# Performance work log

Measured on AMD Instinct MI355X. Metric: run time of the kernel, lower is better.

Reference implementation:

```python
import jax, jax.numpy as jnp
import numpy as np
from jax import lax
from jax.scipy.special import logsumexp

B, T, Lc = 64, 512, 16
DW, CD, NF, KS, H, K, CV = 300, 50, 100, 3, 256, 9, 100
SCALE = 0.05


def setup_inputs() -> dict:
    key = jax.random.key(0)
    ks = jax.random.split(key, 20)
    f32 = jnp.float32
    return {
        'word_embs': jax.random.normal(ks[0], (B, T, DW), f32),
        'chars': jax.random.randint(ks[1], (B, T, Lc), 0, CV),
        'lengths': jax.random.randint(ks[2], (B,), T // 2, T + 1).astype(jnp.int32),
        'tags': jax.random.randint(ks[3], (B, T), 0, K),
        'fin_W': jax.random.normal(ks[4], (DW, DW), f32) * SCALE,
        'fin_b': jnp.zeros((DW,), f32),
        'char_emb': jax.random.normal(ks[5], (CV, CD), f32) * SCALE,
        'conv_W': jax.random.normal(ks[6], (KS, CD, NF), f32) * SCALE,  # (W, In, Out)
        'conv_b': jnp.zeros((NF,), f32),
        'Wih_f': jax.random.normal(ks[7], (4 * H, DW + NF), f32) * SCALE,
        'Whh_f': jax.random.normal(ks[8], (4 * H, H), f32) * SCALE,
        'b_f': jnp.zeros((4 * H,), f32),
        'Wih_b': jax.random.normal(ks[9], (4 * H, DW + NF), f32) * SCALE,
        'Whh_b': jax.random.normal(ks[10], (4 * H, H), f32) * SCALE,
        'b_b': jnp.zeros((4 * H,), f32),
        'out_W': jax.random.normal(ks[11], (2 * H, K), f32) * SCALE,
        'out_b': jnp.zeros((K,), f32),
        'trans': jax.random.normal(ks[12], (K, K), f32) * SCALE,
        'start_trans': jax.random.normal(ks[13], (K,), f32) * SCALE,
        'end_trans': jax.random.normal(ks[14], (K,), f32) * SCALE,
    }


def _lstm_scan(x, mask, Wih, Whh, b):
    # x: [B,T,D], mask: [B,T] bool -> outputs [B,T,H] (zeros at padding)
    xT = jnp.swapaxes(x, 0, 1)              # [T,B,D]
    mT = jnp.swapaxes(mask, 0, 1)           # [T,B]
    pre = jnp.einsum('tbd,gd->tbg', xT, Wih) + b  # precompute input part [T,B,4H]
    h0 = jnp.zeros((x.shape[0], Whh.shape[1]), x.dtype)

    def step(carry, inp):
        h, c = carry
        px, m = inp
        g = px + h @ Whh.T
        i, f, gg, o = jnp.split(g, 4, axis=-1)  # pytorch gate order i,f,g,o
        c_new = jax.nn.sigmoid(f) * c + jax.nn.sigmoid(i) * jnp.tanh(gg)
        h_new = jax.nn.sigmoid(o) * jnp.tanh(c_new)
        m = m[:, None]
        h2 = jnp.where(m, h_new, h)
        c2 = jnp.where(m, c_new, c)
        return (h2, c2), h2 * m

    _, hs = lax.scan(step, (h0, h0), (pre, mT))
    return jnp.swapaxes(hs, 0, 1)


def _reverse_by_length(x, lengths):
    # reverse the valid prefix of each sequence (padding stays at the end)
    t = jnp.arange(x.shape[1])
    rev = jnp.where(t[None, :] < lengths[:, None], lengths[:, None] - 1 - t[None, :], t[None, :])
    return jnp.take_along_axis(x, rev[:, :, None], axis=1)


def _crf_forward(logits, tags, mask, trans, start_trans, end_trans):
    # torchcrf-style log-likelihood; returns scalar sum over batch
    eT = jnp.swapaxes(logits, 0, 1)  # [T,B,K]
    mT = jnp.swapaxes(mask, 0, 1).astype(logits.dtype)  # [T,B]
    bidx = jnp.arange(logits.shape[0])
    # numerator: gold path score
    score = start_trans[tags[:, 0]] + eT[0][bidx, tags[:, 0]]

    def nstep(carry, inp):
        sc, prev = carry
        e, tg, m = inp
        step_sc = trans[prev, tg] + e[bidx, tg]
        sc = sc + m * step_sc
        prev = jnp.where(m > 0, tg, prev)
        return (sc, prev), None

    tT = jnp.swapaxes(tags, 0, 1)
    (score, last_tag), _ = lax.scan(nstep, (score, tags[:, 0]), (eT[1:], tT[1:], mT[1:]))
    score = score + end_trans[last_tag]
    # denominator: log-partition via forward algorithm
    alpha = start_trans[None, :] + eT[0]

    def fstep(a, inp):
        e, m = inp
        nxt = logsumexp(a[:, :, None] + trans[None, :, :] + e[:, None, :], axis=1)
        return jnp.where(m[:, None] > 0, nxt, a), None

    alpha, _ = lax.scan(fstep, alpha, (eT[1:], mT[1:]))
    Z = logsumexp(alpha + end_trans[None, :], axis=-1)
    return jnp.sum(score - Z)


def _viterbi(logits, mask, trans, start_trans, end_trans):
    eT = jnp.swapaxes(logits, 0, 1)  # [T,B,K]
    mT = jnp.swapaxes(mask, 0, 1)    # [T,B] bool
    Ktags = logits.shape[-1]
    ident = jnp.arange(Ktags)[None, :]

    def vstep(a, inp):
        e, m = inp
        cand = a[:, :, None] + trans[None, :, :]   # [B, K_prev, K_cur]
        bp = jnp.argmax(cand, axis=1)
        nxt = jnp.max(cand, axis=1) + e
        a2 = jnp.where(m[:, None], nxt, a)
        bp = jnp.where(m[:, None], bp, ident)       # identity backptr at padding
        return a2, bp

    alpha, bps = lax.scan(vstep, start_trans[None, :] + eT[0], (eT[1:], mT[1:]))
    last = jnp.argmax(alpha + end_trans[None, :], axis=-1)

    def bstep(tag, bp):
        prev = jnp.take_along_axis(bp, tag[:, None], axis=1)[:, 0]
        return prev, tag

    tag0, tail = lax.scan(bstep, last, bps, reverse=True)  # tail[t] = tag at time t+1
    path = jnp.concatenate([tag0[:, None], jnp.swapaxes(tail, 0, 1)], axis=1)  # [B,T]
    return path * mask  # zero-pad like zero_pad(preds)


def reference(word_embs, chars, lengths, tags, fin_W, fin_b, char_emb, conv_W, conv_b,
              Wih_f, Whh_f, b_f, Wih_b, Whh_b, b_b, out_W, out_b,
              trans, start_trans, end_trans):
    mask = jnp.arange(T)[None, :] < lengths[:, None]  # [B,T]
    # 1) word embeddings through finetune linear
    we = word_embs @ fin_W.T + fin_b
    # 2) char CNN: embed -> conv1d over chars -> relu -> max-pool
    ce = char_emb[chars].reshape(B * T, Lc, CD)
    conv = lax.conv_general_dilated(ce, conv_W, (1,), 'SAME',
                                    dimension_numbers=('NWC', 'WIO', 'NWC')) + conv_b
    char_feat = jnp.max(jax.nn.relu(conv), axis=1).reshape(B, T, NF)
    # 3) concat; 4) BiLSTM (dropout=0 / eval mode)
    x = jnp.concatenate([we, char_feat], axis=-1)
    h_fwd = _lstm_scan(x, mask, Wih_f, Whh_f, b_f)
    x_rev = _reverse_by_length(x, lengths)
    h_bwd = _reverse_by_length(_lstm_scan(x_rev, mask, Wih_b, Whh_b, b_b), lengths)
    lstm_out = jnp.concatenate([h_fwd, h_bwd], axis=-1)  # [B,T,2H]
    # 5) linear head; 6-7) CRF loss + viterbi decode
    logits = lstm_out @ out_W + out_b  # [B,T,K]
    loss = -_crf_forward(logits, tags, mask, trans, start_trans, end_trans)
    preds = _viterbi(logits, mask, trans, start_trans, end_trans)
    return loss, preds
```

## Files before the change

### kernel.cpp

```cpp
#include <hip/hip_runtime.h>


__device__ __forceinline__ float sigf(float x){ return 1.0f/(1.0f + expf(-x)); }

__global__ void pack_weights(const float* __restrict__ Wih_f, const float* __restrict__ Wih_b,
                             const float* __restrict__ Whh_f, const float* __restrict__ Whh_b,
                             const float* __restrict__ fin_W,
                             float4* __restrict__ Wp_f, float4* __restrict__ Wp_b,
                             float4* __restrict__ WT_f, float4* __restrict__ WT_b,
                             float* __restrict__ finWT){
  int stride = gridDim.x*blockDim.x;
  for (int idx = blockIdx.x*blockDim.x + threadIdx.x; idx < 425872; idx += stride){
    if (idx < 204800){
      int i2 = idx; const float* W = Wih_f; float4* P = Wp_f;
      if (i2 >= 102400){ i2 -= 102400; W = Wih_b; P = Wp_b; }
      int d = i2 >> 8, j = i2 & 255;
      P[i2] = make_float4(W[j*400+d], W[(j+256)*400+d], W[(j+512)*400+d], W[(j+768)*400+d]);
    } else if (idx < 335872){
      int i2 = idx - 204800; const float* W = Whh_f; float4* P = WT_f;
      if (i2 >= 65536){ i2 -= 65536; W = Whh_b; P = WT_b; }
      int d = i2 >> 8, j = i2 & 255;
      P[i2] = make_float4(W[j*256+d], W[(j+256)*256+d], W[(j+512)*256+d], W[(j+768)*256+d]);
    } else {
      int i2 = idx - 335872;
      int d = i2 / 300, j = i2 - d*300;
      finWT[d*304 + j] = fin_W[j*300 + d];
    }
  }
}

__global__ __launch_bounds__(256) void embed_kernel(const float* __restrict__ we_in,
      const float* __restrict__ finWT, const float* __restrict__ finb, float* __restrict__ x){
  __shared__ float embT[300*16];
  int tok0 = blockIdx.x * 16;
  for (int idx = threadIdx.x; idx < 4800; idx += 256){
    int tt = idx / 300, d = idx - tt*300;
    embT[d*16 + tt] = we_in[(size_t)tok0*300 + idx];
  }
  __syncthreads();
  for (int j = threadIdx.x; j < 300; j += 256){
    float bias = finb[j];
    float acc[16];
#pragma unroll
    for (int k2=0;k2<16;k2++) acc[k2]=bias;
    const float4* e4 = (const float4*)embT;
#pragma unroll 4
    for (int d=0; d<300; d++){
      float w = finWT[d*304 + j];
      float4 a = e4[d*4+0], b2 = e4[d*4+1], c2 = e4[d*4+2], d2 = e4[d*4+3];
      acc[0]+=a.x*w;  acc[1]+=a.y*w;  acc[2]+=a.z*w;  acc[3]+=a.w*w;
      acc[4]+=b2.x*w; acc[5]+=b2.y*w; acc[6]+=b2.z*w; acc[7]+=b2.w*w;
      acc[8]+=c2.x*w; acc[9]+=c2.y*w; acc[10]+=c2.z*w;acc[11]+=c2.w*w;
      acc[12]+=d2.x*w;acc[13]+=d2.y*w;acc[14]+=d2.z*w;acc[15]+=d2.w*w;
    }
#pragma unroll
    for (int k2=0;k2<16;k2++) x[(size_t)(tok0+k2)*400 + j] = acc[k2];
  }
}

__global__ __launch_bounds__(256) void char_kernel(const int* __restrict__ chars,
      const float* __restrict__ char_emb, const float* __restrict__ convW,
      const float* __restrict__ convb, float* __restrict__ x){
  __shared__ float ce2[8*952];
  __shared__ int chs[128];
  int tok0 = blockIdx.x * 8;
  int tid = threadIdx.x;
  if (tid < 128) chs[tid] = chars[(size_t)tok0*16 + tid];
  __syncthreads();
  for (int idx = tid; idx < 7200; idx += 256){
    int tok = idx / 900; int r = idx - tok*900;
    int w1 = r / 50; int c = r - w1*50;
    float v = 0.f;
    if (w1 >= 1 && w1 <= 16) v = char_emb[chs[tok*16 + (w1-1)]*50 + c];
    ce2[tok*952 + c*19 + w1] = v;
  }
  __syncthreads();
  for (int p = tid; p < 800; p += 256){
    int tok = p / 100, f = p - tok*100;
    float s[16];
#pragma unroll
    for (int w=0; w<16; w++) s[w] = 0.f;
    const float* cebase = ce2 + tok*952;
    for (int c=0; c<50; c++){
      float cr[18];
#pragma unroll
      for (int i=0;i<18;i++) cr[i] = cebase[c*19+i];
#pragma unroll
      for (int k2=0;k2<3;k2++){
        float wv = convW[(k2*50+c)*100 + f];
#pragma unroll
        for (int w=0;w<16;w++) s[w] += cr[w+k2]*wv;
      }
    }
    float m = s[0];
#pragma unroll
    for (int w=1;w<16;w++) m = fmaxf(m, s[w]);
    m = fmaxf(0.f, m + convb[f]);
    x[(size_t)(tok0+tok)*400 + 300 + f] = m;
  }
}

__global__ __launch_bounds__(256) void pre_gemm(const float* __restrict__ x,
     const float4* __restrict__ Wp_f, const float4* __restrict__ Wp_b,
     const float* __restrict__ b_f, const float* __restrict__ b_b,
     const int* __restrict__ lengths,
     float4* __restrict__ pre_f, float4* __restrict__ pre_b,
     int t0, int log2CH){
  int dir = blockIdx.z;
  const float4* Wp = dir ? Wp_b : Wp_f;
  const float* bias = dir ? b_b : b_f;
  float4* pre = dir ? pre_b : pre_f;
  int tok0 = blockIdx.x * 64;
  int j0 = blockIdx.y * 64;
  __shared__ float As[16][68];
  __shared__ float4 Bs[4][16][16];
  __shared__ int rows_s[64];
  int tid = threadIdx.x;
  int tx = tid & 15, ty = tid >> 4;
  if (tid < 64){
    int tok = tok0 + tid;
    int b = tok >> log2CH;
    int trel = tok - (b << log2CH);
    int t = t0 + trel;
    int row;
    if (dir == 0) row = t;
    else { int len = lengths[b]; int pr = len - 1 - t; row = pr < 0 ? 0 : pr; }
    rows_s[tid] = b*512 + row;
  }
  float4 acc[4][4];
#pragma unroll
  for (int s2=0;s2<4;s2++){
    int j = j0 + tx*4 + s2;
    float4 bj = make_float4(bias[j], bias[j+256], bias[j+512], bias[j+768]);
#pragma unroll
    for (int r=0;r<4;r++) acc[r][s2] = bj;
  }
  __syncthreads();
  int tokA = tid >> 2, kqA = tid & 3;
  int jjB = tid & 63,  kbB = tid >> 6;
  float4 aReg; float4 bReg[4];
  {
    aReg = *(const float4*)&x[(size_t)rows_s[tokA]*400 + 0 + kqA*4];
#pragma unroll
    for (int rr=0;rr<4;rr++) bReg[rr] = Wp[(size_t)(0 + kbB + rr*4)*256 + j0 + jjB];
  }
  for (int kt=0; kt<25; ++kt){
    As[kqA*4+0][tokA] = aReg.x;
    As[kqA*4+1][tokA] = aReg.y;
    As[kqA*4+2][tokA] = aReg.z;
    As[kqA*4+3][tokA] = aReg.w;
#pragma unroll
    for (int rr=0;rr<4;rr++) Bs[jjB&3][kbB+rr*4][jjB>>2] = bReg[rr];
    __syncthreads();
    if (kt < 24){
      int k0n = (kt+1)*16;
      aReg = *(const float4*)&x[(size_t)rows_s[tokA]*400 + k0n + kqA*4];
#pragma unroll
      for (int rr=0;rr<4;rr++) bReg[rr] = Wp[(size_t)(k0n + kbB + rr*4)*256 + j0 + jjB];
    }
#pragma unroll
    for (int kk=0; kk<16; ++kk){
      float a[4];
#pragma unroll
      for (int r=0;r<4;r++) a[r] = As[kk][ty*4+r];
#pragma unroll
      for (int s2=0;s2<4;s2++){
        float4 b4 = Bs[s2][kk][tx];
#pragma unroll
        for (int r=0;r<4;r++){
          acc[r][s2].x += a[r]*b4.x;
          acc[r][s2].y += a[r]*b4.y;
          acc[r][s2].z += a[r]*b4.z;
          acc[r][s2].w += a[r]*b4.w;
        }
      }
    }
    __syncthreads();
  }
#pragma unroll
  for (int r=0;r<4;r++){
    int tok = tok0 + ty*4 + r;
    int bb = tok >> log2CH;
    int tr = tok - (bb << log2CH);
#pragma unroll
    for (int s2=0;s2<4;s2++){
      pre[(size_t)(bb*128 + tr)*256 + j0 + tx*4 + s2] = acc[r][s2];
    }
  }
}

#define NRD 24
#define NLD 8
#define NSTREAM (64 - NRD - NLD)

#define OFF_WLDS 0
#define OFF_PART 131072
#define OFF_OWS  143360
#define OFF_H    152576
#define POOL_SZ  154624
#define PG_AS    0
#define PG_BS    4352
#define PG_ROWS  12544
#define PG_STRIDE 12800

__global__ __launch_bounds__(1024, 1)
void fused_scan_pre(const float4* __restrict__ prec_f, const float4* __restrict__ prec_b,
     const float4* __restrict__ pren_f, float4* __restrict__ pren_f_w,
     float4* __restrict__ pren_b_w,
     const float4* __restrict__ WT_f, const float4* __restrict__ WT_b,
     const float4* __restrict__ Wp_f, const float4* __restrict__ Wp_b,
     const float* __restrict__ b_f, const float* __restrict__ b_b,
     const float* __restrict__ x, const int* __restrict__ lengths,
     const float* __restrict__ outW,
     float* __restrict__ logits_f, float* __restrict__ logits_b,
     float* __restrict__ st_h, float* __restrict__ st_c,
     int t0, int nsteps, int t0n, int do_pre){
  __shared__ __align__(16) char smem[POOL_SZ];
  int wid = blockIdx.x;
  int tid = threadIdx.x;
  if (wid < 128){
    int dir = wid & 1;
    int b = wid >> 1;
    int len = lengths[b];
    if (len <= t0) return;
    const float4* pre = (dir ? prec_b : prec_f) + (size_t)b*128*256;
    const float4* WT = dir ? WT_b : WT_f;
    float* lg = (dir ? logits_b : logits_f) + (size_t)b*512*9;
    float4* wlds = (float4*)(smem + OFF_WLDS);
    float4* part = (float4*)(smem + OFF_PART);
    float*  oWs  = (float*)(smem + OFF_OWS);
    float*  hbuf = (float*)(smem + OFF_H);
    int j = tid & 255, q = tid >> 8;
    for (int i = tid; i < 2304; i += 1024) oWs[i] = outW[dir*2304 + i];
    for (int i = tid; i < 4*NLD*256; i += 1024){
      int qq = i >> 11;
      int rr = i & (NLD*256 - 1);
      int dl = rr >> 8, jj = rr & 255;
      wlds[(qq*NLD + dl)*256 + jj] = WT[(size_t)(qq*64 + NRD + dl)*256 + jj];
    }
    const float4* WTq = WT + (size_t)q*64*256;
    float4 wreg[NRD];
#pragma unroll
    for (int r=0; r<NRD; ++r) wreg[r] = WTq[(size_t)r*256 + j];
    float c = 0.f;
    if (t0 == 0){
      if (tid < 256) hbuf[tid] = 0.f;
    } else {
      if (tid < 256) hbuf[tid] = st_h[(dir*64+b)*256 + tid];
      if (q == 0) c = st_c[(dir*64+b)*256 + j];
    }
    __syncthreads();
    int tend = len < t0+nsteps ? len : t0+nsteps;
    const float4* WTs = WTq + (size_t)(NRD+NLD)*256 + j;
    int cur = 0;
    for (int t=t0; t<tend; ++t){
      const float* hc = hbuf + (cur << 8);
      const float* hq = hc + (q << 6);
      float4 p0;
      if (q == 0) p0 = pre[(size_t)(t - t0)*256 + j];
      float4 acc = make_float4(0.f,0.f,0.f,0.f);
#pragma unroll 8
      for (int s=0; s<NSTREAM; ++s){
        float hv = hq[NRD+NLD+s];
        float4 w = WTs[(size_t)s*256];
        acc.x += w.x*hv; acc.y += w.y*hv; acc.z += w.z*hv; acc.w += w.w*hv;
      }
#pragma unroll
      for (int r=0; r<NRD; ++r){
        float hv = hq[r];
        float4 w = wreg[r];
        acc.x += w.x*hv; acc.y += w.y*hv; acc.z += w.z*hv; acc.w += w.w*hv;
      }
#pragma unroll
      for (int l=0; l<NLD; ++l){
        float hv = hq[NRD+l];
        float4 w = wlds[(q*NLD + l)*256 + j];
        acc.x += w.x*hv; acc.y += w.y*hv; acc.z += w.z*hv; acc.w += w.w*hv;
      }
      if (q) part[((q-1)<<8) + j] = acc;
      if (t > t0 && tid < 576){
        int pprev = dir ? (len - t) : (t - 1);
        int k = tid >> 6, l = tid & 63;
        float s = hc[l]*oWs[l*9+k] + hc[l+64]*oWs[(l+64)*9+k]
                + hc[l+128]*oWs[(l+128)*9+k] + hc[l+192]*oWs[(l+192)*9+k];
#pragma unroll
        for (int o=32; o; o>>=1) s += __shfl_down(s, o, 64);
        if (l == 0) lg[pprev*9 + k] = s;
      }
      __syncthreads();
      if (q == 0){
        float4 p1 = part[j], p2 = part[256+j], p3 = part[512+j];
        float gi = acc.x + p0.x + p1.x + p2.x + p3.x;
        float gf = acc.y + p0.y + p1.y + p2.y + p3.y;
        float gg = acc.z + p0.z + p1.z + p2.z + p3.z;
        float go = acc.w + p0.w + p1.w + p2.w + p3.w;
        c = sigf(gf)*c + sigf(gi)*tanhf(gg);
        float h = sigf(go)*tanhf(c);
        hbuf[((cur^1)<<8) + j] = h;
      }
      __syncthreads();
      cur ^= 1;
    }
    const float* hc = hbuf + (cur << 8);
    if (tid < 576){
      int plast = dir ? (len - tend) : (tend - 1);
      int k = tid >> 6, l = tid & 63;
      float s = hc[l]*oWs[l*9+k] + hc[l+64]*oWs[(l+64)*9+k]
              + hc[l+128]*oWs[(l+128)*9+k] + hc[l+192]*oWs[(l+192)*9+k];
#pragma unroll
      for (int o=32; o; o>>=1) s += __shfl_down(s, o, 64);
      if (l == 0) lg[plast*9 + k] = s;
    }
    if (tid < 256) st_h[(dir*64+b)*256 + tid] = hc[tid];
    if (q == 0) st_c[(dir*64+b)*256 + j] = c;
  } else {
    if (!do_pre) return;
    int w = wid - 128;
    int g = tid >> 8, lt = tid & 255;
    char* gp = smem + g*PG_STRIDE;
    float (*As)[68] = (float(*)[68])(gp + PG_AS);
    float4* Bsl = (float4*)(gp + PG_BS);
    int* rows = (int*)(gp + PG_ROWS);
    int tx = lt & 15, ty4 = (lt >> 4) * 4;
    int tokA = lt >> 2, kqA = lt & 3;
    int uB = lt & 31, kbB = lt >> 5;
    for (int s=0; s<4; ++s){
      int tix = s*512 + g*128 + w;
      int dir = tix & 1;
      int jh = (tix >> 1) & 7;
      int tokT = tix >> 4;
      int j0u = jh * 32;
      int tok0 = tokT * 64;
      const float4* Wp = dir ? Wp_b : Wp_f;
      const float* bias = dir ? b_b : b_f;
      float4* pren = dir ? pren_b_w : pren_f_w;
      __syncthreads();
      if (lt < 64){
        int tok = tok0 + lt;
        int bb = tok >> 7, trel = tok & 127;
        int t = t0n + trel; if (t > 511) t = 511;
        int row;
        if (dir == 0) row = t;
        else { int len = lengths[bb]; int pr = len - 1 - t; row = pr < 0 ? 0 : pr; }
        rows[lt] = bb*512 + row;
      }
      float4 acc[4][2];
#pragma unroll
      for (int s2=0;s2<2;s2++){
        int u = j0u + tx + s2*16;
        float4 bj = make_float4(bias[u], bias[u+256], bias[u+512], bias[u+768]);
#pragma unroll
        for (int r=0;r<4;r++) acc[r][s2] = bj;
      }
      __syncthreads();
      for (int kt=0; kt<25; ++kt){
        int k0 = kt*16;
        {
          const float* xr = x + (size_t)rows[tokA]*400 + k0 + kqA*4;
          float4 av = *(const float4*)xr;
          As[kqA*4+0][tokA]=av.x; As[kqA*4+1][tokA]=av.y;
          As[kqA*4+2][tokA]=av.z; As[kqA*4+3][tokA]=av.w;
          Bsl[kbB*32 + uB]     = Wp[(size_t)(k0+kbB)*256 + j0u + uB];
          Bsl[(kbB+8)*32 + uB] = Wp[(size_t)(k0+kbB+8)*256 + j0u + uB];
        }
        __syncthreads();
#pragma unroll 4
        for (int kk=0; kk<16; ++kk){
          float a0 = As[kk][ty4+0], a1 = As[kk][ty4+1], a2 = As[kk][ty4+2], a3 = As[kk][ty4+3];
          float4 b0 = Bsl[kk*32 + tx], b1 = Bsl[kk*32 + tx + 16];
          acc[0][0].x += a0*b0.x; acc[0][0].y += a0*b0.y; acc[0][0].z += a0*b0.z; acc[0][0].w += a0*b0.w;
          acc[1][0].x += a1*b0.x; acc[1][0].y += a1*b0.y; acc[1][0].z += a1*b0.z; acc[1][0].w += a1*b0.w;
          acc[2][0].x += a2*b0.x; acc[2][0].y += a2*b0.y; acc[2][0].z += a2*b0.z; acc[2][0].w += a2*b0.w;
          acc[3][0].x += a3*b0.x; acc[3][0].y += a3*b0.y; acc[3][0].z += a3*b0.z; acc[3][0].w += a3*b0.w;
          acc[0][1].x += a0*b1.x; acc[0][1].y += a0*b1.y; acc[0][1].z += a0*b1.z; acc[0][1].w += a0*b1.w;
          acc[1][1].x += a1*b1.x; acc[1][1].y += a1*b1.y; acc[1][1].z += a1*b1.z; acc[1][1].w += a1*b1.w;
          acc[2][1].x += a2*b1.x; acc[2][1].y += a2*b1.y; acc[2][1].z += a2*b1.z; acc[2][1].w += a2*b1.w;
          acc[3][1].x += a3*b1.x; acc[3][1].y += a3*b1.y; acc[3][1].z += a3*b1.z; acc[3][1].w += a3*b1.w;
        }
        __syncthreads();
      }
#pragma unroll
      for (int r=0;r<4;r++){
        int tok = tok0 + ty4 + r;
        pren[(size_t)tok*256 + j0u + tx]      = acc[r][0];
        pren[(size_t)tok*256 + j0u + tx + 16] = acc[r][1];
      }
    }
  }
}

__global__ __launch_bounds__(64) void crf_viterbi_kernel(const float* __restrict__ logits_f,
     const float* __restrict__ logits_b, const float* __restrict__ outb_,
     const int* __restrict__ tags, const int* __restrict__ lengths,
     const float* __restrict__ trans, const float* __restrict__ start_trans,
     const float* __restrict__ end_trans, float* __restrict__ loss_partial,
     float* __restrict__ preds){
  int wid = blockIdx.x;
  int is_crf = wid < 64 ? 1 : 0;
  int b = is_crf ? wid : wid - 64;
  int len = lengths[b];
  int tid = threadIdx.x;
  __shared__ float e_s[4608];
  __shared__ float tr[81];
  __shared__ float alpha[9];
  __shared__ int tg[512];
  __shared__ unsigned char bp[4608];
  const float* lf = logits_f + (size_t)b*4608;
  const float* lb = logits_b + (size_t)b*4608;
  for (int i=tid; i<4608; i+=64){
    int k = i - (i/9)*9;
    e_s[i] = lf[i] + lb[i] + outb_[k];
  }
  for (int i=tid; i<81; i+=64) tr[i] = trans[i];
  if (is_crf){
    for (int i=tid; i<512; i+=64) tg[i] = tags[b*512 + i];
    __syncthreads();
    if (tid < 9) alpha[tid] = start_trans[tid] + e_s[tid];
    __syncthreads();
    for (int t=1; t<len; ++t){
      float nxt = 0.f;
      if (tid < 9){
        float v[9];
#pragma unroll
        for (int j2=0;j2<9;j2++) v[j2] = alpha[j2] + tr[j2*9+tid];
        float m = v[0];
#pragma unroll
        for (int j2=1;j2<9;j2++) m = fmaxf(m, v[j2]);
        float ssum = 0.f;
#pragma unroll
        for (int j2=0;j2<9;j2++) ssum += expf(v[j2]-m);
        nxt = m + logf(ssum) + e_s[t*9+tid];
      }
      __syncthreads();
      if (tid < 9) alpha[tid] = nxt;
      __syncthreads();
    }
    if (tid == 0){
      float m = alpha[0] + end_trans[0];
      for (int k2=1;k2<9;k2++) m = fmaxf(m, alpha[k2]+end_trans[k2]);
      float ssum = 0.f;
      for (int k2=0;k2<9;k2++) ssum += expf(alpha[k2]+end_trans[k2]-m);
      float Z = m + logf(ssum);
      int prev = tg[0];
      float sc = start_trans[prev] + e_s[prev];
      for (int t=1;t<len;++t){
        int cur = tg[t];
        sc += tr[prev*9+cur] + e_s[t*9+cur];
        prev = cur;
      }
      sc += end_trans[prev];
      loss_partial[b] = Z - sc;
    }
  } else {
    __syncthreads();
    if (tid < 9) alpha[tid] = start_trans[tid] + e_s[tid];
    __syncthreads();
    for (int t=1; t<len; ++t){
      float nxt = 0.f; int bj = 0;
      if (tid < 9){
        float m = alpha[0] + tr[tid];
#pragma unroll
        for (int j2=1;j2<9;j2++){
          float v = alpha[j2] + tr[j2*9+tid];
          if (v > m){ m = v; bj = j2; }
        }
        nxt = m + e_s[t*9+tid];
      }
      __syncthreads();
      if (tid < 9){ alpha[tid] = nxt; bp[t*9+tid] = (unsigned char)bj; }
      __syncthreads();
    }
    for (int p2 = len + tid; p2 < 512; p2 += 64) preds[(size_t)b*512 + p2] = 0.f;
    if (tid == 0){
      float m = alpha[0] + end_trans[0]; int last = 0;
      for (int k2=1;k2<9;k2++){
        float v = alpha[k2] + end_trans[k2];
        if (v > m){ m = v; last = k2; }
      }
      int cur = last;
      preds[(size_t)b*512 + (len-1)] = (float)cur;
      for (int p2 = len-2; p2 >= 0; --p2){
        cur = bp[(p2+1)*9 + cur];
        preds[(size_t)b*512 + p2] = (float)cur;
      }
    }
  }
}

__global__ void loss_sum_kernel(const float* __restrict__ lp, float* __restrict__ out){
  float v = lp[threadIdx.x];
#pragma unroll
  for (int o=32; o; o>>=1) v += __shfl_down(v, o, 64);
  if (threadIdx.x == 0) out[0] = v;
}

extern "C" void kernel_launch(void* const* d_in, const int* in_sizes, int n_in,
                              void* d_out, int out_size, void* d_ws, size_t ws_size,
                              hipStream_t stream) {
  const float* word_embs  = (const float*)d_in[0];
  const int*   chars      = (const int*)  d_in[1];
  const int*   lengths    = (const int*)  d_in[2];
  const int*   tags       = (const int*)  d_in[3];
  const float* fin_W      = (const float*)d_in[4];
  const float* fin_b      = (const float*)d_in[5];
  const float* char_emb   = (const float*)d_in[6];
  const float* conv_W     = (const float*)d_in[7];
  const float* conv_b     = (const float*)d_in[8];
  const float* Wih_f      = (const float*)d_in[9];
  const float* Whh_f      = (const float*)d_in[10];
  const float* b_f        = (const float*)d_in[11];
  const float* Wih_b      = (const float*)d_in[12];
  const float* Whh_b      = (const float*)d_in[13];
  const float* b_b        = (const float*)d_in[14];
  const float* out_W      = (const float*)d_in[15];
  const float* out_b      = (const float*)d_in[16];
  const float* trans      = (const float*)d_in[17];
  const float* start_tr   = (const float*)d_in[18];
  const float* end_tr     = (const float*)d_in[19];

  float* ws = (float*)d_ws;
  float*  x         = ws;
  float4* Wp_f      = (float4*)(ws + 13107200);
  float4* Wp_b      = (float4*)(ws + 13516800);
  float4* WT_f      = (float4*)(ws + 13926400);
  float4* WT_b      = (float4*)(ws + 14188544);
  float*  finWT     = ws + 14450688;
  float*  logits_f  = ws + 14541888;
  float*  logits_b  = ws + 14836800;
  float*  st_h      = ws + 15131712;
  float*  st_c      = ws + 15164480;
  float*  loss_part = ws + 15197248;
  const size_t FIXED_F = 15197312;
  float4* preA_f = (float4*)(ws + FIXED_F);
  float4* preA_b = preA_f + (size_t)64*128*256;
  float4* preB_f = preA_b + (size_t)64*128*256;
  float4* preB_b = preB_f + (size_t)64*128*256;

  float* out = (float*)d_out;

  pack_weights<<<1664, 256, 0, stream>>>(Wih_f, Wih_b, Whh_f, Whh_b, fin_W,
                                         Wp_f, Wp_b, WT_f, WT_b, finWT);
  embed_kernel<<<2048, 256, 0, stream>>>(word_embs, finWT, fin_b, x);
  char_kernel<<<4096, 256, 0, stream>>>(chars, char_emb, conv_W, conv_b, x);

  pre_gemm<<<dim3(64, 4, 2), 256, 0, stream>>>(x, Wp_f, Wp_b, b_f, b_b, lengths,
                                               preA_f, preA_b, 0, 6);
  fused_scan_pre<<<256, 1024, 0, stream>>>(preA_f, preA_b, preB_f, preB_f, preB_b,
      WT_f, WT_b, Wp_f, Wp_b, b_f, b_b, x, lengths, out_W,
      logits_f, logits_b, st_h, st_c, 0, 64, 64, 1);
  fused_scan_pre<<<256, 1024, 0, stream>>>(preB_f, preB_b, preA_f, preA_f, preA_b,
      WT_f, WT_b, Wp_f, Wp_b, b_f, b_b, x, lengths, out_W,
      logits_f, logits_b, st_h, st_c, 64, 128, 192, 1);
  fused_scan_pre<<<256, 1024, 0, stream>>>(preA_f, preA_b, preB_f, preB_f, preB_b,
      WT_f, WT_b, Wp_f, Wp_b, b_f, b_b, x, lengths, out_W,
      logits_f, logits_b, st_h, st_c, 192, 128, 320, 1);
  fused_scan_pre<<<256, 1024, 0, stream>>>(preB_f, preB_b, preA_f, preA_f, preA_b,
      WT_f, WT_b, Wp_f, Wp_b, b_f, b_b, x, lengths, out_W,
      logits_f, logits_b, st_h, st_c, 320, 128, 448, 1);
  fused_scan_pre<<<256, 1024, 0, stream>>>(preA_f, preA_b, preB_f, preB_f, preB_b,
      WT_f, WT_b, Wp_f, Wp_b, b_f, b_b, x, lengths, out_W,
      logits_f, logits_b, st_h, st_c, 448, 64, 0, 0);

  crf_viterbi_kernel<<<128, 64, 0, stream>>>(logits_f, logits_b, out_b, tags, lengths,
                                             trans, start_tr, end_tr, loss_part, out + 1);
  loss_sum_kernel<<<1, 64, 0, stream>>>(loss_part, out);
}
```

Baseline: 3.822 ms.

## Merge embed and char kernels, shrink initial chunk, cap scan VGPRs

Combines the word-embedding projection and char CNN into a single featurize launch that dispatches on block index, removing one kernel launch. The first pre-GEMM chunk is halved to 32 timesteps so the serial scan starts sooner, and the remaining chunk boundaries shift accordingly, with the last chunk growing to 96 steps. The fused scan kernel gets an explicit 128-VGPR attribute, which may cause spills. A mask replaces the subtract in the pre_gemm index math.

```diff
diff --git a/kernel.cpp b/kernel.cpp
--- a/kernel.cpp
+++ b/kernel.cpp
@@ -29,74 +29,77 @@
   }
 }
 
-__global__ __launch_bounds__(256) void embed_kernel(const float* __restrict__ we_in,
-      const float* __restrict__ finWT, const float* __restrict__ finb, float* __restrict__ x){
-  __shared__ float embT[300*16];
-  int tok0 = blockIdx.x * 16;
-  for (int idx = threadIdx.x; idx < 4800; idx += 256){
-    int tt = idx / 300, d = idx - tt*300;
-    embT[d*16 + tt] = we_in[(size_t)tok0*300 + idx];
-  }
-  __syncthreads();
-  for (int j = threadIdx.x; j < 300; j += 256){
-    float bias = finb[j];
-    float acc[16];
-#pragma unroll
-    for (int k2=0;k2<16;k2++) acc[k2]=bias;
-    const float4* e4 = (const float4*)embT;
+__global__ __launch_bounds__(256) void featurize(const float* __restrict__ we_in,
+      const float* __restrict__ finWT, const float* __restrict__ finb,
+      const int* __restrict__ chars, const float* __restrict__ char_emb,
+      const float* __restrict__ convW, const float* __restrict__ convb,
+      float* __restrict__ x){
+  __shared__ __align__(16) char fsm[31104];
+  int bid = blockIdx.x;
+  int tid = threadIdx.x;
+  if (bid < 2048){
+    float* embT = (float*)fsm;
+    int tok0 = bid * 16;
+    for (int idx = tid; idx < 4800; idx += 256){
+      int tt = idx / 300, d = idx - tt*300;
+      embT[d*16 + tt] = we_in[(size_t)tok0*300 + idx];
+    }
+    __syncthreads();
+    for (int j = tid; j < 300; j += 256){
+      float bias = finb[j];
+      float acc[16];
+#pragma unroll
+      for (int k2=0;k2<16;k2++) acc[k2]=bias;
+      const float4* e4 = (const float4*)embT;
 #pragma unroll 4
-    for (int d=0; d<300; d++){
-      float w = finWT[d*304 + j];
-      float4 a = e4[d*4+0], b2 = e4[d*4+1], c2 = e4[d*4+2], d2 = e4[d*4+3];
-      acc[0]+=a.x*w;  acc[1]+=a.y*w;  acc[2]+=a.z*w;  acc[3]+=a.w*w;
-      acc[4]+=b2.x*w; acc[5]+=b2.y*w; acc[6]+=b2.z*w; acc[7]+=b2.w*w;
-      acc[8]+=c2.x*w; acc[9]+=c2.y*w; acc[10]+=c2.z*w;acc[11]+=c2.w*w;
-      acc[12]+=d2.x*w;acc[13]+=d2.y*w;acc[14]+=d2.z*w;acc[15]+=d2.w*w;
-    }
-#pragma unroll
-    for (int k2=0;k2<16;k2++) x[(size_t)(tok0+k2)*400 + j] = acc[k2];
-  }
-}
-
-__global__ __launch_bounds__(256) void char_kernel(const int* __restrict__ chars,
-      const float* __restrict__ char_emb, const float* __restrict__ convW,
-      const float* __restrict__ convb, float* __restrict__ x){
-  __shared__ float ce2[8*952];
-  __shared__ int chs[128];
-  int tok0 = blockIdx.x * 8;
-  int tid = threadIdx.x;
-  if (tid < 128) chs[tid] = chars[(size_t)tok0*16 + tid];
-  __syncthreads();
-  for (int idx = tid; idx < 7200; idx += 256){
-    int tok = idx / 900; int r = idx - tok*900;
-    int w1 = r / 50; int c = r - w1*50;
-    float v = 0.f;
-    if (w1 >= 1 && w1 <= 16) v = char_emb[chs[tok*16 + (w1-1)]*50 + c];
-    ce2[tok*952 + c*19 + w1] = v;
-  }
-  __syncthreads();
-  for (int p = tid; p < 800; p += 256){
-    int tok = p / 100, f = p - tok*100;
-    float s[16];
-#pragma unroll
-    for (int w=0; w<16; w++) s[w] = 0.f;
-    const float* cebase = ce2 + tok*952;
-    for (int c=0; c<50; c++){
-      float cr[18];
-#pragma unroll
-      for (int i=0;i<18;i++) cr[i] = cebase[c*19+i];
-#pragma unroll
-      for (int k2=0;k2<3;k2++){
-        float wv = convW[(k2*50+c)*100 + f];
-#pragma unroll
-        for (int w=0;w<16;w++) s[w] += cr[w+k2]*wv;
-      }
-    }
-    float m = s[0];
-#pragma unroll
-    for (int w=1;w<16;w++) m = fmaxf(m, s[w]);
-    m = fmaxf(0.f, m + convb[f]);
-    x[(size_t)(tok0+tok)*400 + 300 + f] = m;
+      for (int d=0; d<300; d++){
+        float w = finWT[d*304 + j];
+        float4 a = e4[d*4+0], b2 = e4[d*4+1], c2 = e4[d*4+2], d2 = e4[d*4+3];
+        acc[0]+=a.x*w;  acc[1]+=a.y*w;  acc[2]+=a.z*w;  acc[3]+=a.w*w;
+        acc[4]+=b2.x*w; acc[5]+=b2.y*w; acc[6]+=b2.z*w; acc[7]+=b2.w*w;
+        acc[8]+=c2.x*w; acc[9]+=c2.y*w; acc[10]+=c2.z*w;acc[11]+=c2.w*w;
+        acc[12]+=d2.x*w;acc[13]+=d2.y*w;acc[14]+=d2.z*w;acc[15]+=d2.w*w;
+      }
+#pragma unroll
+      for (int k2=0;k2<16;k2++) x[(size_t)(tok0+k2)*400 + j] = acc[k2];
+    }
+  } else {
+    float* ce2 = (float*)fsm;
+    int* chs = (int*)(fsm + 30464);
+    int tok0 = (bid - 2048) * 8;
+    if (tid < 128) chs[tid] = chars[(size_t)tok0*16 + tid];
+    __syncthreads();
+    for (int idx = tid; idx < 7200; idx += 256){
+      int tok = idx / 900; int r = idx - tok*900;
+      int w1 = r / 50; int c = r - w1*50;
+      float v = 0.f;
+      if (w1 >= 1 && w1 <= 16) v = char_emb[chs[tok*16 + (w1-1)]*50 + c];
+      ce2[tok*952 + c*19 + w1] = v;
+    }
+    __syncthreads();
+    for (int p = tid; p < 800; p += 256){
+      int tok = p / 100, f = p - tok*100;
+      float s[16];
+#pragma unroll
+      for (int w=0; w<16; w++) s[w] = 0.f;
+      const float* cebase = ce2 + tok*952;
+      for (int c=0; c<50; c++){
+        float cr[18];
+#pragma unroll
+        for (int i=0;i<18;i++) cr[i] = cebase[c*19+i];
+#pragma unroll
+        for (int k2=0;k2<3;k2++){
+          float wv = convW[(k2*50+c)*100 + f];
+#pragma unroll
+          for (int w=0;w<16;w++) s[w] += cr[w+k2]*wv;
+        }
+      }
+      float m = s[0];
+#pragma unroll
+      for (int w=1;w<16;w++) m = fmaxf(m, s[w]);
+      m = fmaxf(0.f, m + convb[f]);
+      x[(size_t)(tok0+tok)*400 + 300 + f] = m;
+    }
   }
 }
 
@@ -117,10 +120,11 @@
   __shared__ int rows_s[64];
   int tid = threadIdx.x;
   int tx = tid & 15, ty = tid >> 4;
+  int chm = (1 << log2CH) - 1;
   if (tid < 64){
     int tok = tok0 + tid;
     int b = tok >> log2CH;
-    int trel = tok - (b << log2CH);
+    int trel = tok & chm;
     int t = t0 + trel;
     int row;
     if (dir == 0) row = t;
@@ -181,7 +185,7 @@
   for (int r=0;r<4;r++){
     int tok = tok0 + ty*4 + r;
     int bb = tok >> log2CH;
-    int tr = tok - (bb << log2CH);
+    int tr = tok & chm;
 #pragma unroll
     for (int s2=0;s2<4;s2++){
       pre[(size_t)(bb*128 + tr)*256 + j0 + tx*4 + s2] = acc[r][s2];
@@ -203,7 +207,7 @@
 #define PG_ROWS  12544
 #define PG_STRIDE 12800
 
-__global__ __launch_bounds__(1024, 1)
+__global__ __attribute__((amdgpu_num_vgpr(128))) __launch_bounds__(1024, 1)
 void fused_scan_pre(const float4* __restrict__ prec_f, const float4* __restrict__ prec_b,
      const float4* __restrict__ pren_f, float4* __restrict__ pren_f_w,
      float4* __restrict__ pren_b_w,
@@ -540,26 +544,26 @@
 
   pack_weights<<<1664, 256, 0, stream>>>(Wih_f, Wih_b, Whh_f, Whh_b, fin_W,
                                          Wp_f, Wp_b, WT_f, WT_b, finWT);
-  embed_kernel<<<2048, 256, 0, stream>>>(word_embs, finWT, fin_b, x);
-  char_kernel<<<4096, 256, 0, stream>>>(chars, char_emb, conv_W, conv_b, x);
-
-  pre_gemm<<<dim3(64, 4, 2), 256, 0, stream>>>(x, Wp_f, Wp_b, b_f, b_b, lengths,
-                                               preA_f, preA_b, 0, 6);
+  featurize<<<6144, 256, 0, stream>>>(word_embs, finWT, fin_b, chars, char_emb,
+                                      conv_W, conv_b, x);
+
+  pre_gemm<<<dim3(32, 4, 2), 256, 0, stream>>>(x, Wp_f, Wp_b, b_f, b_b, lengths,
+                                               preA_f, preA_b, 0, 5);
   fused_scan_pre<<<256, 1024, 0, stream>>>(preA_f, preA_b, preB_f, preB_f, preB_b,
       WT_f, WT_b, Wp_f, Wp_b, b_f, b_b, x, lengths, out_W,
-      logits_f, logits_b, st_h, st_c, 0, 64, 64, 1);
+      logits_f, logits_b, st_h, st_c, 0, 32, 32, 1);
   fused_scan_pre<<<256, 1024, 0, stream>>>(preB_f, preB_b, preA_f, preA_f, preA_b,
       WT_f, WT_b, Wp_f, Wp_b, b_f, b_b, x, lengths, out_W,
-      logits_f, logits_b, st_h, st_c, 64, 128, 192, 1);
+      logits_f, logits_b, st_h, st_c, 32, 128, 160, 1);
   fused_scan_pre<<<256, 1024, 0, stream>>>(preA_f, preA_b, preB_f, preB_f, preB_b,
       WT_f, WT_b, Wp_f, Wp_b, b_f, b_b, x, lengths, out_W,
-      logits_f, logits_b, st_h, st_c, 192, 128, 320, 1);
+      logits_f, logits_b, st_h, st_c, 160, 128, 288, 1);
   fused_scan_pre<<<256, 1024, 0, stream>>>(preB_f, preB_b, preA_f, preA_f, preA_b,
       WT_f, WT_b, Wp_f, Wp_b, b_f, b_b, x, lengths, out_W,
-      logits_f, logits_b, st_h, st_c, 320, 128, 448, 1);
+      logits_f, logits_b, st_h, st_c, 288, 128, 416, 1);
   fused_scan_pre<<<256, 1024, 0, stream>>>(preA_f, preA_b, preB_f, preB_f, preB_b,
       WT_f, WT_b, Wp_f, Wp_b, b_f, b_b, x, lengths, out_W,
-      logits_f, logits_b, st_h, st_c, 448, 64, 0, 0);
+      logits_f, logits_b, st_h, st_c, 416, 96, 0, 0);
 
   crf_viterbi_kernel<<<128, 64, 0, stream>>>(logits_f, logits_b, out_b, tags, lengths,
                                              trans, start_tr, end_tr, loss_part, out + 1);
```

Measured after the change: 3.887 ms. No clear change (+1.7%).
